# Performance work log

Measured on AMD Instinct MI355X. Metric: run time of the kernel, lower is better.

## Reference

```python
import jax, jax.numpy as jnp
import numpy as np

MASK_OUT_VALUE = -10000.0


def setup_inputs() -> dict:
    key = jax.random.key(0)
    k1, k2, k3 = jax.random.split(key, 3)
    B, H, S, D = 2, 16, 2048, 64
    query = jax.random.normal(k1, (B, H, S, D), dtype=jnp.float32)
    key_t = jax.random.normal(k2, (B, H, S, D), dtype=jnp.float32)
    value = jax.random.normal(k3, (B, H, S, D), dtype=jnp.float32)
    # causal mask: (1, 1, S, S), True where attention is allowed
    mask = jnp.tril(jnp.ones((S, S), dtype=bool))[None, None, :, :]
    return {"query": query, "key": key_t, "value": value, "mask": mask}


def reference(query, key, value, mask):
    # scores: (B, H, S, S)
    scale = 1.0 / jnp.sqrt(jnp.asarray(query.shape[-1], query.dtype))
    attn_scores = jnp.einsum("bhqd,bhkd->bhqk", query, key) * scale
    attn_scores = jnp.where(mask, attn_scores,
                            jnp.asarray(MASK_OUT_VALUE, attn_scores.dtype))
    attn_weights = jax.nn.softmax(attn_scores, axis=-1)
    # dropout is identity (p=0 / eval mode)
    attn_output = jnp.einsum("bhqk,bhkd->bhqd", attn_weights, value)
    return attn_output
```

## Files before the change

kernel.cpp:

```cpp
#include <hip/hip_runtime.h>
#include <math.h>


#define S_LEN   2048
#define D_HEAD  64
#define SCALE_L2E 0.18033688011112042f
#define FIXM    8.0f

using bf16x8 = __attribute__((ext_vector_type(8))) short;
using f32x4  = __attribute__((ext_vector_type(4))) float;
using uint4v = __attribute__((ext_vector_type(4))) unsigned int;

__device__ __forceinline__ unsigned int rnd_bf(float f) {
  return __float_as_uint(f) + 0x8000u;
}
__device__ __forceinline__ unsigned short f2bf(float f) {
  return (unsigned short)(rnd_bf(f) >> 16);
}

__device__ __forceinline__ void gl_lds16(const unsigned short* g, unsigned short* l) {
  __builtin_amdgcn_global_load_lds(
      (const __attribute__((address_space(1))) unsigned int*)g,
      (__attribute__((address_space(3))) unsigned int*)l, 16, 0, 0);
}

__device__ __forceinline__ unsigned int cvtpk_bf16(float lo, float hi) {
  unsigned int r;
  asm("v_cvt_pk_bf16_f32 %0, %1, %2" : "=v"(r) : "v"(lo), "v"(hi));
  return r;
}
__device__ __forceinline__ void swap32(unsigned int& a, unsigned int& b) {
  asm("v_permlane32_swap_b32 %0, %1" : "+v"(a), "+v"(b));
}
__device__ __forceinline__ void swap16(unsigned int& a, unsigned int& b) {
  asm("v_permlane16_swap_b32 %0, %1" : "+v"(a), "+v"(b));
}

template <int CTRL>
__device__ __forceinline__ float dppf(float x) {
  return __builtin_bit_cast(float,
      __builtin_amdgcn_update_dpp(0, __builtin_bit_cast(int, x), CTRL, 0xF, 0xF, false));
}
__device__ __forceinline__ float rowsum16(float x) {
  x += dppf<0xB1>(x);
  x += dppf<0x4E>(x);
  x += dppf<0x124>(x);
  x += dppf<0x128>(x);
  return x;
}

__global__ __launch_bounds__(256, 4)
void prep(const float* __restrict__ Kg, const float* __restrict__ Vg,
          unsigned short* __restrict__ Kb, unsigned short* __restrict__ Vt)
{
  __shared__ __align__(16) unsigned short Lt[64][72];
  const int j = blockIdx.x, t = threadIdx.x;
  const int bh = j >> 4, seg = j & 15;
  const size_t base = (size_t)bh * (S_LEN * D_HEAD) + (size_t)seg * 128 * D_HEAD;
#pragma unroll
  for (int i = 0; i < 8; ++i) {
    const size_t idx = base + i * 1024 + t * 4;
    const f32x4 v = *(const f32x4*)(Kg + idx);
    uint2 pk;
    pk.x = (rnd_bf(v[1]) & 0xFFFF0000u) | (rnd_bf(v[0]) >> 16);
    pk.y = (rnd_bf(v[3]) & 0xFFFF0000u) | (rnd_bf(v[2]) >> 16);
    *(uint2*)(Kb + idx) = pk;
  }
  for (int h = 0; h < 2; ++h) {
    const int s0 = seg * 128 + h * 64;
    __syncthreads();
#pragma unroll
    for (int pp = 0; pp < 4; ++pp) {
      const int r = t >> 2;
      const int d0 = (t & 3) * 4 + pp * 16;
      const f32x4 v = *(const f32x4*)(Vg + (size_t)bh * (S_LEN * D_HEAD)
                                         + (size_t)(s0 + r) * D_HEAD + d0);
#pragma unroll
      for (int e = 0; e < 4; ++e) Lt[d0 + e][r] = f2bf(v[e]);
    }
    __syncthreads();
#pragma unroll
    for (int q = 0; q < 2; ++q) {
      const int d = t >> 2, ch = (t & 3) + 4 * q;
      *(uint4*)(Vt + (size_t)(bh * 64 + d) * S_LEN + s0 + ch * 8) =
          *(const uint4*)&Lt[d][ch * 8];
    }
  }
}

__global__ __launch_bounds__(256, 2)
void fa(const float* __restrict__ Qg, const unsigned short* __restrict__ Kb,
        const unsigned short* __restrict__ Vt, float* __restrict__ Og)
{
  __shared__ unsigned short Ks[2][2][64][64];
  __shared__ unsigned short Vs[2][2][64][64];

  const int id = blockIdx.x;
  const int bh = id & 31;
  const int pr = id >> 5;

  const int t    = threadIdx.x;
  const int w    = t >> 6;
  const int lane = t & 63;
  const int c    = lane & 15;
  const int quad = lane >> 4;

  const float* __restrict__ Qb = Qg + (size_t)bh * (S_LEN * D_HEAD);
  float* __restrict__ Ob = Og + (size_t)bh * (S_LEN * D_HEAD);

  const int tr0 = pr, tr1 = 31 - pr;

  int fOff[4][2];
#pragma unroll
  for (int ci = 0; ci < 4; ++ci)
#pragma unroll
    for (int h = 0; h < 2; ++h)
      fOff[ci][h] = ((ci * 16 + c) << 6) + (((h * 4 + quad) ^ (c & 7)) << 3);

  const int rl = lane >> 3;
  const int jj = (lane & 7) ^ rl;
  auto stage1 = [&](int kt, int buf, int sub) {
#pragma unroll
    for (int n = 0; n < 2; ++n) {
      const int row = w * 16 + n * 8 + rl;
      gl_lds16(Kb + (((size_t)(bh * S_LEN + kt * 64 + row)) << 6) + jj * 8,
               &Ks[buf][sub][w * 16 + n * 8][0]);
      gl_lds16(Vt + (((size_t)(bh * 64 + row)) << 11) + kt * 64 + jj * 8,
               &Vs[buf][sub][w * 16 + n * 8][0]);
    }
  };
  auto stage_pair = [&](int it, int tr, int buf) {
    const int k0 = 2 * it;
    stage1(k0, buf, 0);
    if (k0 + 1 <= tr) stage1(k0 + 1, buf, 1);
  };

  bf16x8 qa[2];
  f32x4 oa[4];
  float ls;

  int buf = 0;
  stage_pair(0, tr0, 0);

#pragma unroll 1
  for (int ph = 0; ph < 2; ++ph) {
    const int tr    = ph ? tr1 : tr0;
    const int row0  = tr * 64 + w * 16;
    const int iters = (tr + 2) >> 1;

    {
      const float* qp = Qb + (size_t)(row0 + c) * D_HEAD + quad * 8;
#pragma unroll
      for (int h = 0; h < 2; ++h) {
        f32x4 a0 = *(const f32x4*)(qp + 32 * h);
        f32x4 a1 = *(const f32x4*)(qp + 32 * h + 4);
#pragma unroll
        for (int j = 0; j < 4; ++j) {
          qa[h][j]     = (short)f2bf(a0[j] * SCALE_L2E);
          qa[h][4 + j] = (short)f2bf(a1[j] * SCALE_L2E);
        }
      }
    }
#pragma unroll
    for (int i = 0; i < 4; ++i) oa[i] = (f32x4){0.f, 0.f, 0.f, 0.f};
    ls = 0.f;

#pragma unroll 1
    for (int it = 0; it < iters; ++it) {
      __syncthreads();
      if (it + 1 < iters)  stage_pair(it + 1, tr, buf ^ 1);
      else if (ph == 0)    stage_pair(0, tr1, buf ^ 1);

#pragma unroll
      for (int s = 0; s < 2; ++s) {
        const int kt = 2 * it + s;
        if (kt <= tr) {
          const unsigned short* ksc = &Ks[buf][s][0][0];
          const unsigned short* vsc = &Vs[buf][s][0][0];
          bf16x8 kf[4][2], vf[4][2];
#pragma unroll
          for (int ci = 0; ci < 4; ++ci)
#pragma unroll
            for (int h = 0; h < 2; ++h) {
              kf[ci][h] = *(const bf16x8*)(ksc + fOff[ci][h]);
              vf[ci][h] = *(const bf16x8*)(vsc + fOff[ci][h]);
            }

          __builtin_amdgcn_s_setprio(1);
          f32x4 sc[4];
#pragma unroll
          for (int ci = 0; ci < 4; ++ci) {
            f32x4 acc = (f32x4){-FIXM, -FIXM, -FIXM, -FIXM};
            acc = __builtin_amdgcn_mfma_f32_16x16x32_bf16(kf[ci][0], qa[0], acc, 0, 0, 0);
            acc = __builtin_amdgcn_mfma_f32_16x16x32_bf16(kf[ci][1], qa[1], acc, 0, 0, 0);
            sc[ci] = acc;
          }
          if (kt == tr) {
            const int grow = row0 + c;
#pragma unroll
            for (int ci = 0; ci < 4; ++ci)
#pragma unroll
              for (int r = 0; r < 4; ++r)
                if (kt * 64 + ci * 16 + quad * 4 + r > grow) sc[ci][r] = -1e30f;
          }
          unsigned int Wt[4][2];
#pragma unroll
          for (int ci = 0; ci < 4; ++ci) {
#pragma unroll
            for (int r = 0; r < 4; ++r)
              sc[ci][r] = __builtin_amdgcn_exp2f(sc[ci][r]);
            ls += (sc[ci][0] + sc[ci][1]) + (sc[ci][2] + sc[ci][3]);
            Wt[ci][0] = cvtpk_bf16(sc[ci][0], sc[ci][1]);
            Wt[ci][1] = cvtpk_bf16(sc[ci][2], sc[ci][3]);
          }
          unsigned int a00 = Wt[0][0], a02 = Wt[1][0]; swap32(a00, a02); swap16(a00, a02);
          unsigned int a01 = Wt[0][1], a03 = Wt[1][1]; swap32(a01, a03); swap16(a01, a03);
          unsigned int a10 = Wt[2][0], a12 = Wt[3][0]; swap32(a10, a12); swap16(a10, a12);
          unsigned int a11 = Wt[2][1], a13 = Wt[3][1]; swap32(a11, a13); swap16(a11, a13);
          const bf16x8 pa0 = __builtin_bit_cast(bf16x8, (uint4v){a00, a01, a02, a03});
          const bf16x8 pa1 = __builtin_bit_cast(bf16x8, (uint4v){a10, a11, a12, a13});

#pragma unroll
          for (int ci = 0; ci < 4; ++ci) {
            oa[ci] = __builtin_amdgcn_mfma_f32_16x16x32_bf16(pa0, vf[ci][0], oa[ci], 0, 0, 0);
            oa[ci] = __builtin_amdgcn_mfma_f32_16x16x32_bf16(pa1, vf[ci][1], oa[ci], 0, 0, 0);
          }
          __builtin_amdgcn_s_setprio(0);
        }
      }
      buf ^= 1;
    }

    {
      float tot = ls;
      tot += __shfl_xor(tot, 16, 64);
      tot += __shfl_xor(tot, 32, 64);
      float inv[4];
#pragma unroll
      for (int r = 0; r < 4; ++r)
        inv[r] = 1.0f / __shfl(tot, quad * 4 + r, 64);
#pragma unroll
      for (int ci = 0; ci < 4; ++ci)
#pragma unroll
        for (int r = 0; r < 4; ++r)
          Ob[(size_t)(row0 + quad * 4 + r) * D_HEAD + ci * 16 + c] =
              oa[ci][r] * inv[r];
    }
  }
}

__global__ __launch_bounds__(256, 4)
void fa_fb(const float* __restrict__ Qg, const float* __restrict__ Kg,
           const float* __restrict__ Vg, float* __restrict__ Og)
{
  __shared__ __align__(16) unsigned short Ksh[64][72];
  __shared__ __align__(16) unsigned short Vsh[64][72];
  __shared__ __align__(16) unsigned short Psh[4][16][72];
  const int id = blockIdx.x;
  const int bh = id & 31;
  const int p  = id >> 5;
  const int t    = threadIdx.x;
  const int w    = t >> 6;
  const int lane = t & 63;
  const int c    = lane & 15;
  const int quad = lane >> 4;
  const size_t base = (size_t)bh * (S_LEN * D_HEAD);
  const float* __restrict__ Qb = Qg + base;
  const float* __restrict__ Kb = Kg + base;
  const float* __restrict__ Vb = Vg + base;
  float* __restrict__ Ob = Og + base;
  const int wv   = w & 1;
  const int row0 = (w >= 2) ? (S_LEN - 32 * (p + 1) + 16 * wv) : (32 * p + 16 * wv);
  const int ktdiag = row0 >> 6;
  const int ktmax  = (S_LEN - 1 - 32 * p) >> 6;
  bf16x8 qa[2];
  {
    const float* qp = Qb + (size_t)(row0 + c) * D_HEAD + quad * 8;
#pragma unroll
    for (int h = 0; h < 2; ++h) {
      f32x4 a0 = *(const f32x4*)(qp + 32 * h);
      f32x4 a1 = *(const f32x4*)(qp + 32 * h + 4);
#pragma unroll
      for (int j = 0; j < 4; ++j) {
        qa[h][j]     = (short)f2bf(a0[j] * SCALE_L2E);
        qa[h][4 + j] = (short)f2bf(a1[j] * SCALE_L2E);
      }
    }
  }
  f32x4 oa[4];
  float ls[4];
#pragma unroll
  for (int i = 0; i < 4; ++i) {
    oa[i] = (f32x4){0.f, 0.f, 0.f, 0.f};
    ls[i] = 0.f;
  }
  for (int kt = 0; kt <= ktmax; ++kt) {
    __syncthreads();
    {
      const int cp = t & 15;
      const int rg = t >> 4;
      const int col0 = cp * 4;
      const int sw = (cp >> 2) << 3;
#pragma unroll
      for (int i = 0; i < 4; ++i) {
        const int row = i * 16 + rg;
        const size_t goff = (size_t)(kt * 64 + row) * D_HEAD + col0;
        const f32x4 kv = *(const f32x4*)(Kb + goff);
        const f32x4 vv = *(const f32x4*)(Vb + goff);
        const unsigned int k01 = (rnd_bf(kv[1]) & 0xFFFF0000u) | (rnd_bf(kv[0]) >> 16);
        const unsigned int k23 = (rnd_bf(kv[3]) & 0xFFFF0000u) | (rnd_bf(kv[2]) >> 16);
        *(uint2*)&Ksh[row][col0] = make_uint2(k01, k23);
        const int kz = row ^ sw;
#pragma unroll
        for (int e = 0; e < 4; ++e)
          Vsh[col0 + e][kz] = f2bf(vv[e]);
      }
    }
    __syncthreads();
    if (kt <= ktdiag) {
      bf16x8 kf[4][2], vf[4][2];
#pragma unroll
      for (int ci = 0; ci < 4; ++ci) {
        kf[ci][0] = *(const bf16x8*)&Ksh[ci * 16 + c][quad * 8];
        kf[ci][1] = *(const bf16x8*)&Ksh[ci * 16 + c][32 + quad * 8];
        vf[ci][0] = *(const bf16x8*)&Vsh[ci * 16 + c][(quad ^ ci) * 8];
        vf[ci][1] = *(const bf16x8*)&Vsh[ci * 16 + c][32 + ((quad ^ ci) * 8)];
      }
      f32x4 sc[4];
#pragma unroll
      for (int ci = 0; ci < 4; ++ci) {
        f32x4 acc = (f32x4){-FIXM, -FIXM, -FIXM, -FIXM};
        acc = __builtin_amdgcn_mfma_f32_16x16x32_bf16(qa[0], kf[ci][0], acc, 0, 0, 0);
        acc = __builtin_amdgcn_mfma_f32_16x16x32_bf16(qa[1], kf[ci][1], acc, 0, 0, 0);
        sc[ci] = acc;
      }
      if (kt == ktdiag) {
#pragma unroll
        for (int ci = 0; ci < 4; ++ci) {
          const int gcol = kt * 64 + ci * 16 + c;
#pragma unroll
          for (int r = 0; r < 4; ++r)
            if (gcol > row0 + quad * 4 + r) sc[ci][r] = -1e30f;
        }
      }
#pragma unroll
      for (int ci = 0; ci < 4; ++ci)
#pragma unroll
        for (int r = 0; r < 4; ++r)
          sc[ci][r] = __builtin_amdgcn_exp2f(sc[ci][r]);
#pragma unroll
      for (int r = 0; r < 4; ++r)
        ls[r] += (sc[0][r] + sc[1][r]) + (sc[2][r] + sc[3][r]);
#pragma unroll
      for (int ci = 0; ci < 4; ++ci)
#pragma unroll
        for (int r = 0; r < 4; ++r) {
          const int prow = quad * 4 + r;
          Psh[w][prow][(ci * 16 + c) ^ ((prow >> 3) << 3)] = f2bf(sc[ci][r]);
        }
      const int px = (c >> 3) << 3;
      const bf16x8 pa0 = *(const bf16x8*)&Psh[w][c][(quad * 8) ^ px];
      const bf16x8 pa1 = *(const bf16x8*)&Psh[w][c][((32 + quad * 8)) ^ px];
#pragma unroll
      for (int ci = 0; ci < 4; ++ci) {
        oa[ci] = __builtin_amdgcn_mfma_f32_16x16x32_bf16(pa0, vf[ci][0], oa[ci], 0, 0, 0);
        oa[ci] = __builtin_amdgcn_mfma_f32_16x16x32_bf16(pa1, vf[ci][1], oa[ci], 0, 0, 0);
      }
    }
  }
  {
    float inv[4];
#pragma unroll
    for (int r = 0; r < 4; ++r) inv[r] = 1.0f / rowsum16(ls[r]);
#pragma unroll
    for (int ci = 0; ci < 4; ++ci)
#pragma unroll
      for (int r = 0; r < 4; ++r)
        Ob[(size_t)(row0 + quad * 4 + r) * D_HEAD + ci * 16 + c] = oa[ci][r] * inv[r];
  }
}

extern "C" void kernel_launch(void* const* d_in, const int* in_sizes, int n_in,
                              void* d_out, int out_size, void* d_ws, size_t ws_size,
                              hipStream_t stream) {
  (void)in_sizes; (void)n_in; (void)out_size;
  const float* Q = (const float*)d_in[0];
  const float* K = (const float*)d_in[1];
  const float* V = (const float*)d_in[2];
  float* O = (float*)d_out;
  const size_t NEED = 2ull * 32 * S_LEN * D_HEAD * 2;
  if (ws_size >= NEED) {
    unsigned short* Kb = (unsigned short*)d_ws;
    unsigned short* Vt = Kb + (size_t)32 * S_LEN * D_HEAD;
    prep<<<dim3(512), dim3(256), 0, stream>>>(K, V, Kb, Vt);
    fa<<<dim3(512), dim3(256), 0, stream>>>(Q, Kb, Vt, O);
  } else {
    fa_fb<<<dim3(1024), dim3(256), 0, stream>>>(Q, K, V, O);
  }
}
```

Before: 131.5 us.

## Interleave two key tiles per iteration and compute row sums via MFMA with ones

The inner loop now loads K fragments for both sub-tiles, issues both QK^T MFMA groups, then loads V and applies masking and exp. This gives the scheduler more independent work to overlap LDS reads, MFMA and transcendental ops. The softmax denominator is now an extra MFMA of the bf16 probabilities against a vector of ones, replacing the scalar adds and the final cross-lane shuffles. In exchange it raises register pressure from holding two tiles' fragments, and the row sum is computed from bf16-rounded weights rather than fp32 values.

```diff
diff --git a/kernel.cpp b/kernel.cpp
--- a/kernel.cpp
+++ b/kernel.cpp
@@ -117,6 +117,10 @@
     for (int h = 0; h < 2; ++h)
       fOff[ci][h] = ((ci * 16 + c) << 6) + (((h * 4 + quad) ^ (c & 7)) << 3);
 
+  bf16x8 ones;
+#pragma unroll
+  for (int j = 0; j < 8; ++j) ones[j] = (short)0x3F80;
+
   const int rl = lane >> 3;
   const int jj = (lane & 7) ^ rl;
   auto stage1 = [&](int kt, int buf, int sub) {
@@ -135,9 +139,27 @@
     if (k0 + 1 <= tr) stage1(k0 + 1, buf, 1);
   };
 
+  auto smpack = [&](f32x4* sc, bf16x8& p0, bf16x8& p1) {
+    unsigned int Wt[4][2];
+#pragma unroll
+    for (int ci = 0; ci < 4; ++ci) {
+#pragma unroll
+      for (int r = 0; r < 4; ++r)
+        sc[ci][r] = __builtin_amdgcn_exp2f(sc[ci][r]);
+      Wt[ci][0] = cvtpk_bf16(sc[ci][0], sc[ci][1]);
+      Wt[ci][1] = cvtpk_bf16(sc[ci][2], sc[ci][3]);
+    }
+    unsigned int a00 = Wt[0][0], a02 = Wt[1][0]; swap32(a00, a02); swap16(a00, a02);
+    unsigned int a01 = Wt[0][1], a03 = Wt[1][1]; swap32(a01, a03); swap16(a01, a03);
+    unsigned int a10 = Wt[2][0], a12 = Wt[3][0]; swap32(a10, a12); swap16(a10, a12);
+    unsigned int a11 = Wt[2][1], a13 = Wt[3][1]; swap32(a11, a13); swap16(a11, a13);
+    p0 = __builtin_bit_cast(bf16x8, (uint4v){a00, a01, a02, a03});
+    p1 = __builtin_bit_cast(bf16x8, (uint4v){a10, a11, a12, a13});
+  };
+
   bf16x8 qa[2];
   f32x4 oa[4];
-  float ls;
+  f32x4 lacc;
 
   int buf = 0;
   stage_pair(0, tr0, 0);
@@ -163,7 +185,7 @@
     }
 #pragma unroll
     for (int i = 0; i < 4; ++i) oa[i] = (f32x4){0.f, 0.f, 0.f, 0.f};
-    ls = 0.f;
+    lacc = (f32x4){0.f, 0.f, 0.f, 0.f};
 
 #pragma unroll 1
     for (int it = 0; it < iters; ++it) {
@@ -171,74 +193,103 @@
       if (it + 1 < iters)  stage_pair(it + 1, tr, buf ^ 1);
       else if (ph == 0)    stage_pair(0, tr1, buf ^ 1);
 
-#pragma unroll
-      for (int s = 0; s < 2; ++s) {
-        const int kt = 2 * it + s;
-        if (kt <= tr) {
-          const unsigned short* ksc = &Ks[buf][s][0][0];
-          const unsigned short* vsc = &Vs[buf][s][0][0];
-          bf16x8 kf[4][2], vf[4][2];
-#pragma unroll
-          for (int ci = 0; ci < 4; ++ci)
-#pragma unroll
-            for (int h = 0; h < 2; ++h) {
-              kf[ci][h] = *(const bf16x8*)(ksc + fOff[ci][h]);
-              vf[ci][h] = *(const bf16x8*)(vsc + fOff[ci][h]);
-            }
-
-          __builtin_amdgcn_s_setprio(1);
-          f32x4 sc[4];
-#pragma unroll
-          for (int ci = 0; ci < 4; ++ci) {
-            f32x4 acc = (f32x4){-FIXM, -FIXM, -FIXM, -FIXM};
-            acc = __builtin_amdgcn_mfma_f32_16x16x32_bf16(kf[ci][0], qa[0], acc, 0, 0, 0);
-            acc = __builtin_amdgcn_mfma_f32_16x16x32_bf16(kf[ci][1], qa[1], acc, 0, 0, 0);
-            sc[ci] = acc;
-          }
-          if (kt == tr) {
-            const int grow = row0 + c;
-#pragma unroll
-            for (int ci = 0; ci < 4; ++ci)
-#pragma unroll
-              for (int r = 0; r < 4; ++r)
-                if (kt * 64 + ci * 16 + quad * 4 + r > grow) sc[ci][r] = -1e30f;
-          }
-          unsigned int Wt[4][2];
-#pragma unroll
-          for (int ci = 0; ci < 4; ++ci) {
-#pragma unroll
-            for (int r = 0; r < 4; ++r)
-              sc[ci][r] = __builtin_amdgcn_exp2f(sc[ci][r]);
-            ls += (sc[ci][0] + sc[ci][1]) + (sc[ci][2] + sc[ci][3]);
-            Wt[ci][0] = cvtpk_bf16(sc[ci][0], sc[ci][1]);
-            Wt[ci][1] = cvtpk_bf16(sc[ci][2], sc[ci][3]);
-          }
-          unsigned int a00 = Wt[0][0], a02 = Wt[1][0]; swap32(a00, a02); swap16(a00, a02);
-          unsigned int a01 = Wt[0][1], a03 = Wt[1][1]; swap32(a01, a03); swap16(a01, a03);
-          unsigned int a10 = Wt[2][0], a12 = Wt[3][0]; swap32(a10, a12); swap16(a10, a12);
-          unsigned int a11 = Wt[2][1], a13 = Wt[3][1]; swap32(a11, a13); swap16(a11, a13);
-          const bf16x8 pa0 = __builtin_bit_cast(bf16x8, (uint4v){a00, a01, a02, a03});
-          const bf16x8 pa1 = __builtin_bit_cast(bf16x8, (uint4v){a10, a11, a12, a13});
-
-#pragma unroll
-          for (int ci = 0; ci < 4; ++ci) {
-            oa[ci] = __builtin_amdgcn_mfma_f32_16x16x32_bf16(pa0, vf[ci][0], oa[ci], 0, 0, 0);
-            oa[ci] = __builtin_amdgcn_mfma_f32_16x16x32_bf16(pa1, vf[ci][1], oa[ci], 0, 0, 0);
-          }
-          __builtin_amdgcn_s_setprio(0);
+      const int kt0 = 2 * it, kt1 = kt0 + 1;
+      const bool has1 = (kt1 <= tr);
+
+      const unsigned short* ks0 = &Ks[buf][0][0][0];
+      const unsigned short* ks1 = &Ks[buf][1][0][0];
+      bf16x8 kf0[4][2], kf1[4][2];
+#pragma unroll
+      for (int ci = 0; ci < 4; ++ci)
+#pragma unroll
+        for (int h = 0; h < 2; ++h)
+          kf0[ci][h] = *(const bf16x8*)(ks0 + fOff[ci][h]);
+      if (has1)
+#pragma unroll
+        for (int ci = 0; ci < 4; ++ci)
+#pragma unroll
+          for (int h = 0; h < 2; ++h)
+            kf1[ci][h] = *(const bf16x8*)(ks1 + fOff[ci][h]);
+
+      __builtin_amdgcn_s_setprio(1);
+      f32x4 sc0[4], sc1[4];
+#pragma unroll
+      for (int ci = 0; ci < 4; ++ci) {
+        f32x4 acc = (f32x4){-FIXM, -FIXM, -FIXM, -FIXM};
+        acc = __builtin_amdgcn_mfma_f32_16x16x32_bf16(kf0[ci][0], qa[0], acc, 0, 0, 0);
+        acc = __builtin_amdgcn_mfma_f32_16x16x32_bf16(kf0[ci][1], qa[1], acc, 0, 0, 0);
+        sc0[ci] = acc;
+      }
+      if (has1)
+#pragma unroll
+        for (int ci = 0; ci < 4; ++ci) {
+          f32x4 acc = (f32x4){-FIXM, -FIXM, -FIXM, -FIXM};
+          acc = __builtin_amdgcn_mfma_f32_16x16x32_bf16(kf1[ci][0], qa[0], acc, 0, 0, 0);
+          acc = __builtin_amdgcn_mfma_f32_16x16x32_bf16(kf1[ci][1], qa[1], acc, 0, 0, 0);
+          sc1[ci] = acc;
         }
-      }
+
+      const unsigned short* vs0 = &Vs[buf][0][0][0];
+      const unsigned short* vs1 = &Vs[buf][1][0][0];
+      bf16x8 vf0[4][2], vf1[4][2];
+#pragma unroll
+      for (int ci = 0; ci < 4; ++ci)
+#pragma unroll
+        for (int h = 0; h < 2; ++h)
+          vf0[ci][h] = *(const bf16x8*)(vs0 + fOff[ci][h]);
+      if (has1)
+#pragma unroll
+        for (int ci = 0; ci < 4; ++ci)
+#pragma unroll
+          for (int h = 0; h < 2; ++h)
+            vf1[ci][h] = *(const bf16x8*)(vs1 + fOff[ci][h]);
+
+      if (kt0 == tr) {
+        const int grow = row0 + c;
+#pragma unroll
+        for (int ci = 0; ci < 4; ++ci)
+#pragma unroll
+          for (int r = 0; r < 4; ++r)
+            if (kt0 * 64 + ci * 16 + quad * 4 + r > grow) sc0[ci][r] = -1e30f;
+      }
+      if (has1 && kt1 == tr) {
+        const int grow = row0 + c;
+#pragma unroll
+        for (int ci = 0; ci < 4; ++ci)
+#pragma unroll
+          for (int r = 0; r < 4; ++r)
+            if (kt1 * 64 + ci * 16 + quad * 4 + r > grow) sc1[ci][r] = -1e30f;
+      }
+
+      bf16x8 paA0, paA1, paB0, paB1;
+      smpack(sc0, paA0, paA1);
+      if (has1) smpack(sc1, paB0, paB1);
+
+#pragma unroll
+      for (int ci = 0; ci < 4; ++ci) {
+        oa[ci] = __builtin_amdgcn_mfma_f32_16x16x32_bf16(paA0, vf0[ci][0], oa[ci], 0, 0, 0);
+        oa[ci] = __builtin_amdgcn_mfma_f32_16x16x32_bf16(paA1, vf0[ci][1], oa[ci], 0, 0, 0);
+      }
+      lacc = __builtin_amdgcn_mfma_f32_16x16x32_bf16(paA0, ones, lacc, 0, 0, 0);
+      lacc = __builtin_amdgcn_mfma_f32_16x16x32_bf16(paA1, ones, lacc, 0, 0, 0);
+      if (has1) {
+#pragma unroll
+        for (int ci = 0; ci < 4; ++ci) {
+          oa[ci] = __builtin_amdgcn_mfma_f32_16x16x32_bf16(paB0, vf1[ci][0], oa[ci], 0, 0, 0);
+          oa[ci] = __builtin_amdgcn_mfma_f32_16x16x32_bf16(paB1, vf1[ci][1], oa[ci], 0, 0, 0);
+        }
+        lacc = __builtin_amdgcn_mfma_f32_16x16x32_bf16(paB0, ones, lacc, 0, 0, 0);
+        lacc = __builtin_amdgcn_mfma_f32_16x16x32_bf16(paB1, ones, lacc, 0, 0, 0);
+      }
+      __builtin_amdgcn_s_setprio(0);
+
       buf ^= 1;
     }
 
     {
-      float tot = ls;
-      tot += __shfl_xor(tot, 16, 64);
-      tot += __shfl_xor(tot, 32, 64);
       float inv[4];
 #pragma unroll
-      for (int r = 0; r < 4; ++r)
-        inv[r] = 1.0f / __shfl(tot, quad * 4 + r, 64);
+      for (int r = 0; r < 4; ++r) inv[r] = 1.0f / lacc[r];
 #pragma unroll
       for (int ci = 0; ci < 4; ++ci)
 #pragma unroll
```

Result: no change. 130.8 us (-0.6%).
